# Kernel tuning notes

Hardware: AMD Instinct MI355X
Metric: run time of the kernel (lower is better)

## Reference

```python
import jax, jax.numpy as jnp
import numpy as np

# Default DigitCaps config: reduced_votes=False, iter=1, softmax=False, tanh_like=False,
# l_thetas=[1.0], lr_som=1.0, radical=False, no normalization, no winner-ratio bookkeeping.
H, Wd, INPUT_F, INPUT_D = 12, 12, 32, 8
C, D, M = 10, 8, 4          # num_out_caps, vector_depth, transf_mat_for_each_caps
LR, THETA = 1.0, 1.0


def setup_inputs() -> dict:
    key = jax.random.key(0)
    k1, k2, k3 = jax.random.split(key, 3)
    B = 128
    inputs = jax.random.normal(k1, (B, H, Wd, INPUT_F, INPUT_D), dtype=jnp.float32)
    J = H * Wd * INPUT_F  # 4608 positions
    # he_normal over fan_in = INPUT_D
    W = jax.random.normal(k2, (J, INPUT_D, D * M), dtype=jnp.float32) * jnp.sqrt(2.0 / INPUT_D)
    digit_caps = jax.random.uniform(k3, (C, D), minval=-1.0, maxval=1.0, dtype=jnp.float32)
    return {"inputs": inputs, "W": W, "digit_caps": digit_caps}


def reference(inputs, W, digit_caps):
    B = inputs.shape[0]
    J = H * Wd * INPUT_F
    x = inputs.reshape(B, J, INPUT_D)
    # per-position transform: [B,J,input_d] x [J,input_d,D*M] -> [B,J,D*M]
    u = jnp.einsum('bji,jik->bjk', x, W)
    N = J * M
    u = u.reshape(B, N, D)  # votes (broadcast over C instead of tiling)

    # similarities[b,n,c] = <u[b,n], digit_caps[c]>
    sims = jnp.einsum('bnd,cd->bnc', u, digit_caps)
    winners = jnp.argmax(sims, axis=-1)  # [B, N] int

    # sparse_updates = one_hot(winners) * (u - digit_caps) * lr * theta;
    # updates = mean over (B, N). Computed via segment-sum (honors winner sparsity).
    flat_w = winners.reshape(-1)
    flat_u = u.reshape(-1, D)
    seg_u = jax.ops.segment_sum(flat_u, flat_w, num_segments=C)          # [C, D]
    counts = jnp.zeros((C,), jnp.float32).at[flat_w].add(1.0)            # [C]
    denom = jnp.float32(B * N)
    updates = (seg_u - counts[:, None] * digit_caps) * (LR * THETA) / denom

    digit_caps_new = digit_caps + updates  # assign_add happens before final sims

    sims_final = jnp.einsum('bnd,cd->bnc', u, digit_caps_new)
    output = jnp.mean(sims_final, axis=-2)  # [B, C]
    return output, digit_caps_new
```

## Files before the change

### kernel.cpp

```cpp
#include <hip/hip_runtime.h>


#define J_POS 4608
#define SEGSTRIDE 97
#define NSEG 32
#define SSTRIDE 520
#define NSREP 8
#define NVOTES 18432.0f
#define DENOM  2359296.0f
#define SEG_SCALE 32768.0f
#define INV_SEG_SCALE 3.0517578125e-5f
#define P2 32
#define ROWS_PER 36

__global__ __launch_bounds__(256) void votes_kernel(
    const float* __restrict__ x,
    const float* __restrict__ w,
    const float* __restrict__ dc,
    int* __restrict__ part_seg,
    int* __restrict__ part_s,
    int* __restrict__ done)
{
    __shared__ int seg_lds[NSEG * SEGSTRIDE];
    __shared__ int s_lds[NSREP * SSTRIDE];

    const int t  = threadIdx.x;
    const int jg = blockIdx.x >> 1;
    const int h  = blockIdx.x & 1;
    const int j0 = jg * 8;

    if (blockIdx.x == 0 && t == 0) *done = 0;

    for (int i = t; i < NSEG * SEGSTRIDE; i += 256) seg_lds[i] = 0;
    for (int i = t; i < NSREP * SSTRIDE; i += 256) s_lds[i] = 0;

    const int jj   = t >> 5;
    const int m    = (t >> 3) & 3;
    const int brow = t & 7;
    const int j = j0 + jj;

    float4 wra[8], wrb[8];
    {
        const float* wp = w + (size_t)j * 256 + m * 8;
        #pragma unroll
        for (int i = 0; i < 8; ++i) {
            wra[i] = *(const float4*)(wp + i * 32);
            wrb[i] = *(const float4*)(wp + i * 32 + 4);
        }
    }

    float dcs[80];
    #pragma unroll
    for (int c = 0; c < 10; ++c) {
        const float4 a = *(const float4*)(dc + c * 8);
        const float4 b = *(const float4*)(dc + c * 8 + 4);
        dcs[c*8+0] = __uint_as_float(__builtin_amdgcn_readfirstlane(__float_as_uint(a.x)));
        dcs[c*8+1] = __uint_as_float(__builtin_amdgcn_readfirstlane(__float_as_uint(a.y)));
        dcs[c*8+2] = __uint_as_float(__builtin_amdgcn_readfirstlane(__float_as_uint(a.z)));
        dcs[c*8+3] = __uint_as_float(__builtin_amdgcn_readfirstlane(__float_as_uint(a.w)));
        dcs[c*8+4] = __uint_as_float(__builtin_amdgcn_readfirstlane(__float_as_uint(b.x)));
        dcs[c*8+5] = __uint_as_float(__builtin_amdgcn_readfirstlane(__float_as_uint(b.y)));
        dcs[c*8+6] = __uint_as_float(__builtin_amdgcn_readfirstlane(__float_as_uint(b.z)));
        dcs[c*8+7] = __uint_as_float(__builtin_amdgcn_readfirstlane(__float_as_uint(b.w)));
    }

    int* const segp = &seg_lds[((t >> 1) & (NSEG - 1)) * SEGSTRIDE];
    int* const sp = &s_lds[((t >> 3) & (NSREP - 1)) * SSTRIDE];

    __syncthreads();

    const float* xp0 = x + ((size_t)(h * 64 + brow) * J_POS + j) * 8;
    float4 nx0 = *(const float4*)xp0;
    float4 nx1 = *(const float4*)(xp0 + 4);

    #pragma unroll 1
    for (int it = 0; it < 8; ++it) {
        const int bl = it * 8 + brow;
        const float4 x0 = nx0, x1 = nx1;
        if (it < 7) {
            const float* xp = x + ((size_t)(h * 64 + bl + 8) * J_POS + j) * 8;
            nx0 = *(const float4*)xp;
            nx1 = *(const float4*)(xp + 4);
        }
        const float xf[8] = {x0.x,x0.y,x0.z,x0.w,x1.x,x1.y,x1.z,x1.w};

        float u[8] = {0,0,0,0,0,0,0,0};
        #pragma unroll
        for (int i = 0; i < 8; ++i) {
            const float xi = xf[i];
            u[0] += xi * wra[i].x; u[1] += xi * wra[i].y;
            u[2] += xi * wra[i].z; u[3] += xi * wra[i].w;
            u[4] += xi * wrb[i].x; u[5] += xi * wrb[i].y;
            u[6] += xi * wrb[i].z; u[7] += xi * wrb[i].w;
        }

        float best = -3.402823466e38f;
        int bc = 0;
        #pragma unroll
        for (int c = 0; c < 10; ++c) {
            const float sim = u[0]*dcs[c*8+0] + u[1]*dcs[c*8+1]
                            + u[2]*dcs[c*8+2] + u[3]*dcs[c*8+3]
                            + u[4]*dcs[c*8+4] + u[5]*dcs[c*8+5]
                            + u[6]*dcs[c*8+6] + u[7]*dcs[c*8+7];
            if (sim > best) { best = sim; bc = c; }
        }

        const int o = bc * 9;
        const int sb = bl * 8;
        #pragma unroll
        for (int d = 0; d < 8; ++d) {
            const int q = __float2int_rn(u[d] * SEG_SCALE);
            atomicAdd(&segp[o + d], q);
            atomicAdd(&sp[sb + d], q);
        }
        atomicAdd(&segp[o + 8], 1);
    }

    __syncthreads();

    if (t < 90) {
        int v = 0;
        #pragma unroll
        for (int r = 0; r < NSEG; ++r) v += seg_lds[r * SEGSTRIDE + t];
        part_seg[blockIdx.x * 96 + t] = v;
    }
    #pragma unroll
    for (int e = t; e < 512; e += 256) {
        int v = 0;
        #pragma unroll
        for (int r = 0; r < NSREP; ++r) v += s_lds[r * SSTRIDE + e];
        part_s[(size_t)blockIdx.x * 512 + e] = v;
    }
}

__global__ __launch_bounds__(256) void reduce_final_kernel(
    const int* __restrict__ part_seg,
    const int* __restrict__ part_s,
    int* __restrict__ part2_s,
    long long* __restrict__ part2_seg,
    int* __restrict__ done,
    const float* __restrict__ dc,
    float* __restrict__ out)
{
    __shared__ float sf[1024];
    __shared__ float dcn[80];
    __shared__ int lastflag;

    const int t = threadIdx.x;
    const int p = blockIdx.x;
    const int r0 = p * ROWS_PER;

    int aE0 = 0, aE1 = 0, aO0 = 0, aO1 = 0;
    #pragma unroll
    for (int i = 0; i < ROWS_PER; ++i) {
        const int2 v = *(const int2*)(part_s + (size_t)(r0 + i) * 512 + 2 * t);
        if (i & 1) { aO0 += v.x; aO1 += v.y; }
        else       { aE0 += v.x; aE1 += v.y; }
    }
    __hip_atomic_store(&part2_s[p * 1024 + 2 * t],       aE0, __ATOMIC_RELAXED, __HIP_MEMORY_SCOPE_AGENT);
    __hip_atomic_store(&part2_s[p * 1024 + 2 * t + 1],   aE1, __ATOMIC_RELAXED, __HIP_MEMORY_SCOPE_AGENT);
    __hip_atomic_store(&part2_s[p * 1024 + 512 + 2 * t],     aO0, __ATOMIC_RELAXED, __HIP_MEMORY_SCOPE_AGENT);
    __hip_atomic_store(&part2_s[p * 1024 + 512 + 2 * t + 1], aO1, __ATOMIC_RELAXED, __HIP_MEMORY_SCOPE_AGENT);

    if (t < 96) {
        long long acc = 0;
        #pragma unroll
        for (int i = 0; i < ROWS_PER; ++i)
            acc += part_seg[(size_t)(r0 + i) * 96 + t];
        __hip_atomic_store(&part2_seg[p * 96 + t], acc,
                           __ATOMIC_RELAXED, __HIP_MEMORY_SCOPE_AGENT);
    }

    __threadfence();
    __syncthreads();
    if (t == 0) lastflag = (atomicAdd(done, 1) == P2 - 1) ? 1 : 0;
    __syncthreads();
    if (!lastflag) return;
    __threadfence();

    #pragma unroll
    for (int g = 0; g < 2; ++g) {
        const int c0 = g * 512 + 2 * t;
        int t0 = 0, t1 = 0;
        #pragma unroll
        for (int q = 0; q < P2; ++q) {
            t0 += __hip_atomic_load(&part2_s[q * 1024 + c0],     __ATOMIC_RELAXED, __HIP_MEMORY_SCOPE_AGENT);
            t1 += __hip_atomic_load(&part2_s[q * 1024 + c0 + 1], __ATOMIC_RELAXED, __HIP_MEMORY_SCOPE_AGENT);
        }
        sf[c0]     = ((float)t0 * INV_SEG_SCALE) * (1.0f / NVOTES);
        sf[c0 + 1] = ((float)t1 * INV_SEG_SCALE) * (1.0f / NVOTES);
    }

    if (t < 80) {
        const int c = t >> 3, d = t & 7;
        long long sv = 0, cv = 0;
        #pragma unroll
        for (int q = 0; q < P2; ++q) {
            sv += __hip_atomic_load(&part2_seg[q * 96 + c * 9 + d], __ATOMIC_RELAXED, __HIP_MEMORY_SCOPE_AGENT);
            cv += __hip_atomic_load(&part2_seg[q * 96 + c * 9 + 8], __ATOMIC_RELAXED, __HIP_MEMORY_SCOPE_AGENT);
        }
        const float d0 = dc[t];
        const float nd = d0 + ((float)sv * INV_SEG_SCALE - (float)cv * d0) * (1.0f / DENOM);
        dcn[t] = nd;
        out[1280 + t] = nd;
    }
    __syncthreads();

    #pragma unroll
    for (int r = 0; r < 5; ++r) {
        const int idx = r * 256 + t;
        const int b = idx / 10, c = idx - b * 10;
        float acc = 0.f;
        #pragma unroll
        for (int d = 0; d < 8; ++d) acc += sf[b * 8 + d] * dcn[c * 8 + d];
        out[idx] = acc;
    }
}

extern "C" void kernel_launch(void* const* d_in, const int* in_sizes, int n_in,
                              void* d_out, int out_size, void* d_ws, size_t ws_size,
                              hipStream_t stream) {
    const float* x  = (const float*)d_in[0];
    const float* w  = (const float*)d_in[1];
    const float* dc = (const float*)d_in[2];
    float* out = (float*)d_out;
    int*       done      = (int*)d_ws;
    long long* part2_seg = (long long*)((char*)d_ws + 64);
    int*       part2_s   = (int*)((char*)d_ws + 24640);
    int*       part_seg  = (int*)((char*)d_ws + 155712);
    int*       part_s    = (int*)((char*)d_ws + 598080);

    votes_kernel<<<1152, 256, 0, stream>>>(x, w, dc, part_seg, part_s, done);
    reduce_final_kernel<<<P2, 256, 0, stream>>>(part_seg, part_s, part2_s,
                                                part2_seg, done, dc, out);
}
```

Before: 101.4 us.

## Stage x and W tiles through LDS with coalesced loads before vote computation

Each block now loads its 8-position W slice and its 64x8-position x tile into shared memory with fully coalesced float4 loads, and threads then read their operands from LDS instead of issuing strided global loads with per-iteration prefetch. The digit-caps values are kept as plain float4 registers instead of being forced into scalar registers with readfirstlane. The goal is to cut uncoalesced global traffic. In exchange it uses more shared memory per block, which may lower occupancy, and it drops the software prefetch overlap.

```diff
diff --git a/kernel.cpp b/kernel.cpp
--- a/kernel.cpp
+++ b/kernel.cpp
@@ -6,6 +6,7 @@
 #define NSEG 32
 #define SSTRIDE 520
 #define NSREP 8
+#define XSTRIDE 68
 #define NVOTES 18432.0f
 #define DENOM  2359296.0f
 #define SEG_SCALE 32768.0f
@@ -21,8 +22,10 @@
     int* __restrict__ part_s,
     int* __restrict__ done)
 {
-    __shared__ int seg_lds[NSEG * SEGSTRIDE];
-    __shared__ int s_lds[NSREP * SSTRIDE];
+    __shared__ int   seg_lds[NSEG * SEGSTRIDE];
+    __shared__ int   s_lds[NSREP * SSTRIDE];
+    __shared__ float x_lds[64 * XSTRIDE];
+    __shared__ float w_lds[2048];
 
     const int t  = threadIdx.x;
     const int jg = blockIdx.x >> 1;
@@ -34,14 +37,43 @@
     for (int i = t; i < NSEG * SEGSTRIDE; i += 256) seg_lds[i] = 0;
     for (int i = t; i < NSREP * SSTRIDE; i += 256) s_lds[i] = 0;
 
+    {
+        const float* wsrc = w + (size_t)j0 * 256;
+        #pragma unroll
+        for (int rep = 0; rep < 2; ++rep) {
+            const int f4 = rep * 256 + t;
+            *(float4*)&w_lds[f4 * 4] = *(const float4*)(wsrc + f4 * 4);
+        }
+    }
+    {
+        #pragma unroll
+        for (int rep = 0; rep < 4; ++rep) {
+            const int idx = rep * 256 + t;
+            const int row = idx >> 4, f4 = idx & 15;
+            *(float4*)&x_lds[row * XSTRIDE + f4 * 4] =
+                *(const float4*)(x + ((size_t)(h * 64 + row) * J_POS + j0) * 8 + f4 * 4);
+        }
+    }
+
     const int jj   = t >> 5;
     const int m    = (t >> 3) & 3;
     const int brow = t & 7;
-    const int j = j0 + jj;
+
+    float4 dca[10], dcb[10];
+    #pragma unroll
+    for (int c = 0; c < 10; ++c) {
+        dca[c] = *(const float4*)(dc + c * 8);
+        dcb[c] = *(const float4*)(dc + c * 8 + 4);
+    }
+
+    int* const segp = &seg_lds[((t >> 1) & (NSEG - 1)) * SEGSTRIDE];
+    int* const sp = &s_lds[((t >> 3) & (NSREP - 1)) * SSTRIDE];
+
+    __syncthreads();
 
     float4 wra[8], wrb[8];
     {
-        const float* wp = w + (size_t)j * 256 + m * 8;
+        const float* wp = &w_lds[jj * 256 + m * 8];
         #pragma unroll
         for (int i = 0; i < 8; ++i) {
             wra[i] = *(const float4*)(wp + i * 32);
@@ -49,39 +81,11 @@
         }
     }
 
-    float dcs[80];
-    #pragma unroll
-    for (int c = 0; c < 10; ++c) {
-        const float4 a = *(const float4*)(dc + c * 8);
-        const float4 b = *(const float4*)(dc + c * 8 + 4);
-        dcs[c*8+0] = __uint_as_float(__builtin_amdgcn_readfirstlane(__float_as_uint(a.x)));
-        dcs[c*8+1] = __uint_as_float(__builtin_amdgcn_readfirstlane(__float_as_uint(a.y)));
-        dcs[c*8+2] = __uint_as_float(__builtin_amdgcn_readfirstlane(__float_as_uint(a.z)));
-        dcs[c*8+3] = __uint_as_float(__builtin_amdgcn_readfirstlane(__float_as_uint(a.w)));
-        dcs[c*8+4] = __uint_as_float(__builtin_amdgcn_readfirstlane(__float_as_uint(b.x)));
-        dcs[c*8+5] = __uint_as_float(__builtin_amdgcn_readfirstlane(__float_as_uint(b.y)));
-        dcs[c*8+6] = __uint_as_float(__builtin_amdgcn_readfirstlane(__float_as_uint(b.z)));
-        dcs[c*8+7] = __uint_as_float(__builtin_amdgcn_readfirstlane(__float_as_uint(b.w)));
-    }
-
-    int* const segp = &seg_lds[((t >> 1) & (NSEG - 1)) * SEGSTRIDE];
-    int* const sp = &s_lds[((t >> 3) & (NSREP - 1)) * SSTRIDE];
-
-    __syncthreads();
-
-    const float* xp0 = x + ((size_t)(h * 64 + brow) * J_POS + j) * 8;
-    float4 nx0 = *(const float4*)xp0;
-    float4 nx1 = *(const float4*)(xp0 + 4);
-
     #pragma unroll 1
     for (int it = 0; it < 8; ++it) {
         const int bl = it * 8 + brow;
-        const float4 x0 = nx0, x1 = nx1;
-        if (it < 7) {
-            const float* xp = x + ((size_t)(h * 64 + bl + 8) * J_POS + j) * 8;
-            nx0 = *(const float4*)xp;
-            nx1 = *(const float4*)(xp + 4);
-        }
+        const float4 x0 = *(const float4*)&x_lds[bl * XSTRIDE + jj * 8];
+        const float4 x1 = *(const float4*)&x_lds[bl * XSTRIDE + jj * 8 + 4];
         const float xf[8] = {x0.x,x0.y,x0.z,x0.w,x1.x,x1.y,x1.z,x1.w};
 
         float u[8] = {0,0,0,0,0,0,0,0};
@@ -98,10 +102,8 @@
         int bc = 0;
         #pragma unroll
         for (int c = 0; c < 10; ++c) {
-            const float sim = u[0]*dcs[c*8+0] + u[1]*dcs[c*8+1]
-                            + u[2]*dcs[c*8+2] + u[3]*dcs[c*8+3]
-                            + u[4]*dcs[c*8+4] + u[5]*dcs[c*8+5]
-                            + u[6]*dcs[c*8+6] + u[7]*dcs[c*8+7];
+            const float sim = u[0]*dca[c].x + u[1]*dca[c].y + u[2]*dca[c].z + u[3]*dca[c].w
+                            + u[4]*dcb[c].x + u[5]*dcb[c].y + u[6]*dcb[c].z + u[7]*dcb[c].w;
             if (sim > best) { best = sim; bc = c; }
         }
 
```

Measured after the change: 106.0 us. 4.6% more time.
